# Kernel tuning notes

Hardware: AMD Instinct MI355X
Metric: run time of the kernel (lower is better)

Reference implementation:

```python
import jax, jax.numpy as jnp
import numpy as np

DIM = 8          # per-head dim
ATT_EPS = 1e-15
BN_EPS = 1e-6


def setup_inputs() -> dict:
    key = jax.random.key(0)
    ks = jax.random.split(key, 6)
    B, C, H, W = 8, 256, 64, 64
    td = 256                      # heads * dim = 32 * 8
    return {
        'x':      jax.random.normal(ks[0], (B, C, H, W), jnp.float32),
        'w_qkv':  jax.random.normal(ks[1], (3 * td, C), jnp.float32) * 0.05,
        'w_dw':   jax.random.normal(ks[2], (3 * td, 1, 5, 5), jnp.float32) * 0.05,
        'w_pw':   jax.random.normal(ks[3], (96, 8, 8), jnp.float32) * 0.05,   # (groups, out/g, in/g)
        'w_proj': jax.random.normal(ks[4], (C, 2 * td), jnp.float32) * 0.05,
        'bn_gamma': jnp.ones((C,), jnp.float32),
        'bn_beta':  jnp.zeros((C,), jnp.float32),
        'bn_mean':  jnp.zeros((C,), jnp.float32),
        'bn_var':   jnp.ones((C,), jnp.float32),
    }


def _relu_linear_att(ms, H, W):
    # ms: [B, C, H, W] with C = heads * 3*DIM
    B = ms.shape[0]
    d = DIM
    qkv = ms.reshape(B, -1, 3 * d, H * W).transpose(0, 1, 3, 2)   # [B, h, N, 3d]
    q = jax.nn.relu(qkv[..., :d])
    k = jax.nn.relu(qkv[..., d:2 * d])
    v = qkv[..., 2 * d:]
    v = jnp.pad(v, ((0, 0), (0, 0), (0, 0), (0, 1)), constant_values=1.0)  # ones column
    kv = jnp.einsum('bhnd,bhne->bhde', k, v)                       # [B, h, d, d+1]
    out = jnp.einsum('bhnd,bhde->bhne', q, kv)                     # [B, h, N, d+1]
    out = out[..., :-1] / (out[..., -1:] + ATT_EPS)
    return out.transpose(0, 1, 3, 2).reshape(B, -1, H, W)          # [B, h*d, H, W]


def reference(x, w_qkv, w_dw, w_pw, w_proj, bn_gamma, bn_beta, bn_mean, bn_var):
    B, C, H, W = x.shape
    # 1x1 qkv projection
    qkv = jnp.einsum('oc,bchw->bohw', w_qkv, x)                    # [B, 768, H, W]
    # multiscale aggregation: 5x5 depthwise then grouped 1x1 (groups = 3*heads = 96)
    dw = jax.lax.conv_general_dilated(
        qkv, w_dw, window_strides=(1, 1), padding=[(2, 2), (2, 2)],
        dimension_numbers=('NCHW', 'OIHW', 'NCHW'),
        feature_group_count=qkv.shape[1])
    G, O, I = w_pw.shape
    agg = jnp.einsum('goi,bgihw->bgohw', w_pw,
                     dw.reshape(B, G, I, H, W)).reshape(B, G * O, H, W)
    ms = jnp.concatenate([qkv, agg], axis=1)                       # [B, 1536, H, W]
    att = _relu_linear_att(ms, H, W)                               # [B, 512, H, W]
    # proj: 1x1 conv + BatchNorm (eval mode) + identity activation
    p = jnp.einsum('oc,bchw->bohw', w_proj, att)                   # [B, 256, H, W]
    inv = bn_gamma / jnp.sqrt(bn_var + BN_EPS)
    p = p * inv[None, :, None, None] + (bn_beta - bn_mean * inv)[None, :, None, None]
    return x + p
```

## Files before the change

### kernel.cpp

```cpp
#include <hip/hip_runtime.h>
#include <hip/hip_bf16.h>


#define HW 4096
#define ATT_EPS 1e-15f
#define BN_EPS 1e-6f

typedef __attribute__((ext_vector_type(8))) short short8;
typedef __attribute__((ext_vector_type(4))) short short4v;
typedef __attribute__((ext_vector_type(4))) float f32x4;
typedef __attribute__((ext_vector_type(2))) float f32x2;
typedef __attribute__((ext_vector_type(8))) unsigned short u16x8;
typedef __attribute__((ext_vector_type(4))) unsigned short u16x4;

static __device__ inline short f2bf(float f) {
    union { float f; unsigned u; } v; v.f = f;
    unsigned r = v.u + 0x7fff + ((v.u >> 16) & 1);
    return (short)(r >> 16);
}
static __device__ inline float bf2f(unsigned short u) {
    union { unsigned u; float f; } v; v.u = (unsigned)u << 16; return v.f;
}

static __device__ inline float dpp_shr1(float x) {
    int i = __builtin_bit_cast(int, x);
    int r = __builtin_amdgcn_update_dpp(0, i, 0x111, 0xF, 0xF, true);
    return __builtin_bit_cast(float, r);
}
static __device__ inline float dpp_shl1(float x) {
    int i = __builtin_bit_cast(int, x);
    int r = __builtin_amdgcn_update_dpp(0, i, 0x101, 0xF, 0xF, true);
    return __builtin_bit_cast(float, r);
}

__global__ __launch_bounds__(256) void prep_w(const float* __restrict__ wproj,
                                              unsigned short* __restrict__ wbf) {
    const int i = (blockIdx.x * 256 + threadIdx.x) * 4;
    float4 v = *(const float4*)&wproj[i];
    u16x4 r = {(unsigned short)f2bf(v.x), (unsigned short)f2bf(v.y),
               (unsigned short)f2bf(v.z), (unsigned short)f2bf(v.w)};
    *(u16x4*)&wbf[i] = r;
}

__global__ __launch_bounds__(256) void prep_wq(const float* __restrict__ wqkv,
                                               unsigned short* __restrict__ wqbf) {
    const int i = (blockIdx.x * 256 + threadIdx.x) * 4;
    float4 v = *(const float4*)&wqkv[i];
    u16x4 r = {(unsigned short)f2bf(v.x), (unsigned short)f2bf(v.y),
               (unsigned short)f2bf(v.z), (unsigned short)f2bf(v.w)};
    *(u16x4*)&wqbf[i] = r;
}

__global__ __launch_bounds__(256) void prep_xt(const float* __restrict__ x,
                                               unsigned short* __restrict__ xt) {
    __shared__ unsigned short tl[64][72];
    const int b = blockIdx.z;
    const int c0 = blockIdx.y * 64, n0 = blockIdx.x * 64;
    const int t = threadIdx.x;
    const int nq = t & 15, cl = t >> 4;
#pragma unroll
    for (int p = 0; p < 4; p++) {
        const int c = cl + p * 16;
        float4 v = *(const float4*)&x[((size_t)b * 256 + c0 + c) * HW + n0 + nq * 4];
        tl[nq * 4 + 0][c] = (unsigned short)f2bf(v.x);
        tl[nq * 4 + 1][c] = (unsigned short)f2bf(v.y);
        tl[nq * 4 + 2][c] = (unsigned short)f2bf(v.z);
        tl[nq * 4 + 3][c] = (unsigned short)f2bf(v.w);
    }
    __syncthreads();
#pragma unroll
    for (int k = 0; k < 2; k++) {
        const int slot = t + 256 * k;
        const int nl = slot >> 3, oct = slot & 7;
        u16x8 v = *(const u16x8*)&tl[nl][oct * 8];
        *(u16x8*)&xt[((size_t)b * 4096 + n0 + nl) * 256 + c0 + oct * 8] = v;
    }
}

__global__ __launch_bounds__(256) void qkv_gemm(const unsigned short* __restrict__ xt,
                                                const unsigned short* __restrict__ wqbf,
                                                unsigned short* __restrict__ qkv) {
    __shared__ unsigned short A_l[128 * 40];
    __shared__ unsigned short B_l[128 * 40];
    const int t  = threadIdx.x;
    const int b  = blockIdx.z;
    const int ob = blockIdx.y * 128;
    const int nb = blockIdx.x * 128;
    const int lane = t & 63, wave = t >> 6;
    const int wo = (wave >> 1) * 64, wn = (wave & 1) * 64;
    const int am = lane & 15, ak = lane >> 4;

    const int r0 = t >> 2, c0 = t & 3;
    const unsigned short* asrc = wqbf + (size_t)(ob + r0) * 256 + c0 * 8;
    const unsigned short* bsrc = xt + ((size_t)b * 4096 + nb + r0) * 256 + c0 * 8;

    f32x4 acc[4][4];
#pragma unroll
    for (int s = 0; s < 4; s++)
#pragma unroll
        for (int u = 0; u < 4; u++) acc[s][u] = (f32x4){0.f, 0.f, 0.f, 0.f};

    for (int kb = 0; kb < 256; kb += 32) {
        __syncthreads();
        *(u16x8*)&A_l[r0 * 40 + c0 * 8] = *(const u16x8*)(asrc + kb);
        *(u16x8*)&A_l[(r0 + 64) * 40 + c0 * 8] =
            *(const u16x8*)(asrc + (size_t)64 * 256 + kb);
        *(u16x8*)&B_l[r0 * 40 + c0 * 8] = *(const u16x8*)(bsrc + kb);
        *(u16x8*)&B_l[(r0 + 64) * 40 + c0 * 8] =
            *(const u16x8*)(bsrc + (size_t)64 * 256 + kb);
        __syncthreads();

        short8 af[4], bf[4];
#pragma unroll
        for (int s = 0; s < 4; s++)
            af[s] = *(const short8*)&A_l[(wo + s * 16 + am) * 40 + ak * 8];
#pragma unroll
        for (int u = 0; u < 4; u++)
            bf[u] = *(const short8*)&B_l[(wn + u * 16 + am) * 40 + ak * 8];
#pragma unroll
        for (int s = 0; s < 4; s++)
#pragma unroll
            for (int u = 0; u < 4; u++)
                acc[s][u] = __builtin_amdgcn_mfma_f32_16x16x32_bf16(af[s], bf[u], acc[s][u], 0, 0, 0);
    }

#pragma unroll
    for (int s = 0; s < 4; s++)
#pragma unroll
        for (int u = 0; u < 4; u++)
#pragma unroll
            for (int r = 0; r < 4; r++) {
                const int o = ob + wo + s * 16 + (lane >> 4) * 4 + r;
                const int nn = nb + wn + u * 16 + (lane & 15);
                qkv[((size_t)b * 768 + o) * HW + nn] = (unsigned short)f2bf(acc[s][u][r]);
            }
}

__global__ __launch_bounds__(256, 6) void dw_agg(const unsigned short* __restrict__ qkv,
                                                 const float* __restrict__ wdw,
                                                 const float* __restrict__ wpw,
                                                 unsigned short* __restrict__ agg) {
    __shared__ float tile[4 * 20 * 64];
    const int b = blockIdx.z, g = blockIdx.y;
    const int y0 = blockIdx.x * 16;
    const int t = threadIdx.x;
    const int tx = t & 15, ty = t >> 4;

    const float* wkg = wdw + g * 8 * 25;
    const float* pwg = wpw + g * 64;

    float out[8][4];
#pragma unroll
    for (int o = 0; o < 8; o++)
#pragma unroll
        for (int j = 0; j < 4; j++) out[o][j] = 0.f;

#pragma unroll 1
    for (int half = 0; half < 2; half++) {
        if (half) __syncthreads();
#pragma unroll
        for (int k = 0; k < 3; k++) {
            const int i = t + 256 * k;
            if (i < 640) {
                const int c8 = i & 7, rr = (i >> 3) % 20, ch = i / 160;
                const int y = y0 - 2 + rr;
                u16x8 v = {0, 0, 0, 0, 0, 0, 0, 0};
                if (y >= 0 && y < 64)
                    v = *(const u16x8*)&qkv[((size_t)(b * 768 + g * 8 + half * 4 + ch)) * HW + y * 64 + c8 * 8];
                f32x4 lo = {bf2f(v[0]), bf2f(v[1]), bf2f(v[2]), bf2f(v[3])};
                f32x4 hi = {bf2f(v[4]), bf2f(v[5]), bf2f(v[6]), bf2f(v[7])};
                *(f32x4*)&tile[i * 8]     = lo;
                *(f32x4*)&tile[i * 8 + 4] = hi;
            }
        }
        __syncthreads();

#pragma unroll 1
        for (int ch4 = 0; ch4 < 4; ch4++) {
            const int ch = half * 4 + ch4;
            const float* wkc = wkg + ch * 25;
            float a0 = 0.f, a1 = 0.f, a2 = 0.f, a3 = 0.f;
#pragma unroll
            for (int dy = 0; dy < 5; dy++) {
                const int off = ch4 * 1280 + (ty + dy) * 64 + tx * 4;
                f32x4 C = *(const f32x4*)&tile[off];
                float win[8];
                win[0] = dpp_shr1(C[2]);
                win[1] = dpp_shr1(C[3]);
                win[2] = C[0]; win[3] = C[1];
                win[4] = C[2]; win[5] = C[3];
                win[6] = dpp_shl1(C[0]);
                win[7] = dpp_shl1(C[1]);
#pragma unroll
                for (int dx = 0; dx < 5; dx++) {
                    const float wv = wkc[dy * 5 + dx];
                    a0 += wv * win[dx + 0];
                    a1 += wv * win[dx + 1];
                    a2 += wv * win[dx + 2];
                    a3 += wv * win[dx + 3];
                }
            }
#pragma unroll
            for (int o = 0; o < 8; o++) {
                const float wv = pwg[o * 8 + ch];
                out[o][0] += wv * a0; out[o][1] += wv * a1;
                out[o][2] += wv * a2; out[o][3] += wv * a3;
            }
        }
    }

#pragma unroll
    for (int o = 0; o < 8; o++) {
        u16x4 rv = {(unsigned short)f2bf(out[o][0]), (unsigned short)f2bf(out[o][1]),
                    (unsigned short)f2bf(out[o][2]), (unsigned short)f2bf(out[o][3])};
        *(u16x4*)&agg[((size_t)(b * 768 + g * 8 + o)) * HW + (y0 + ty) * 64 + tx * 4] = rv;
    }
}

__global__ __launch_bounds__(256) void kv_pass(const unsigned short* __restrict__ qkv,
                                               const unsigned short* __restrict__ agg,
                                               float* __restrict__ kvpart) {
    const int t = threadIdx.x;
    const int w = t >> 6, lane = t & 63;
    const int hp = blockIdx.x * 4 + w;
    const int b = blockIdx.y, c = blockIdx.z;
    const int h0 = hp * 2, h1 = h0 + 1;
    const unsigned short* buf = (h0 < 32) ? qkv : agg;
    const int cb0 = (h0 & 31) * 24, cb1 = (h1 & 31) * 24;

    const int row = lane & 15, kgrp = lane >> 4;
    const int n0 = c * 256 + kgrp * 8;

    const int chA = (row < 8) ? (cb0 + 8 + row) : (cb1 + row);
    const unsigned short* ap = buf + ((size_t)b * 768 + chA) * HW + n0;

    const bool bload = (row < 8);
    const unsigned short* bp0 = buf + ((size_t)b * 768 + cb0 + 16 + (row & 7)) * HW + n0;
    const unsigned short* bp1 = buf + ((size_t)b * 768 + cb1 + 16 + (row & 7)) * HW + n0;
    const short cfill = (row == 8) ? (short)0x3F80 : (short)0;
    const short8 bconst = {cfill, cfill, cfill, cfill, cfill, cfill, cfill, cfill};

    f32x4 acc0 = {0.f, 0.f, 0.f, 0.f};
    f32x4 acc1 = {0.f, 0.f, 0.f, 0.f};

#pragma unroll
    for (int i = 0; i < 8; i++) {
        u16x8 av = *(const u16x8*)(ap + i * 32);
        short8 b0 = bload ? *(const short8*)(bp0 + i * 32) : bconst;
        short8 b1 = bload ? *(const short8*)(bp1 + i * 32) : bconst;
        short8 ar;
#pragma unroll
        for (int j = 0; j < 8; j++)
            ar[j] = (short)((av[j] & 0x8000) ? 0 : av[j]);
        acc0 = __builtin_amdgcn_mfma_f32_16x16x32_bf16(ar, b0, acc0, 0, 0, 0);
        acc1 = __builtin_amdgcn_mfma_f32_16x16x32_bf16(ar, b1, acc1, 0, 0, 0);
    }

    if (row <= 8) {
        float* kp;
        f32x4 a;
        int dbase;
        if (kgrp < 2) {
            kp = kvpart + (size_t)c * 36864 + (size_t)(b * 64 + h0) * 72;
            a = acc0; dbase = kgrp * 4;
        } else {
            kp = kvpart + (size_t)c * 36864 + (size_t)(b * 64 + h1) * 72;
            a = acc1; dbase = (kgrp - 2) * 4;
        }
#pragma unroll
        for (int r = 0; r < 4; r++)
            kp[(dbase + r) * 9 + row] = a[r];
    }
}

__global__ __launch_bounds__(256) void kv_red(const float* __restrict__ kvpart,
                                              float* __restrict__ kvout) {
    const int i = blockIdx.x * 256 + threadIdx.x;
    float s = 0.f;
#pragma unroll
    for (int c = 0; c < 16; c++) s += kvpart[(size_t)c * 36864 + i];
    kvout[i] = s;
}

__global__ __launch_bounds__(256) void att_pass(const unsigned short* __restrict__ qkv,
                                                const unsigned short* __restrict__ agg,
                                                const float* __restrict__ kvbuf,
                                                unsigned short* __restrict__ att_f) {
    const int h = blockIdx.y, b = blockIdx.z;
    const int t = threadIdx.x;
    const float* kvp = kvbuf + ((size_t)(b * 64 + h)) * 72;

    float kvr[72];
#pragma unroll
    for (int i = 0; i < 18; i++) {
        f32x4 v = *(const f32x4*)&kvp[i * 4];
        kvr[i * 4 + 0] = v[0]; kvr[i * 4 + 1] = v[1];
        kvr[i * 4 + 2] = v[2]; kvr[i * 4 + 3] = v[3];
    }

    const unsigned short* buf = (h < 32) ? qkv : agg;
    const int cbase = (h & 31) * 24;
    const int n0 = (blockIdx.x * 256 + t) * 8;
    const unsigned short* qp = buf + ((size_t)b * 768 + cbase) * HW + n0;

    float q[8][8];
#pragma unroll
    for (int d = 0; d < 8; d++) {
        u16x8 v = *(const u16x8*)&qp[(size_t)d * HW];
#pragma unroll
        for (int j = 0; j < 8; j++) q[d][j] = fmaxf(bf2f(v[j]), 0.f);
    }

    unsigned short* op = att_f + (((size_t)(b * 64 + h)) * HW + n0) * 8;
#pragma unroll
    for (int j = 0; j < 8; j++) {
        float num[9];
#pragma unroll
        for (int e = 0; e < 9; e++) num[e] = 0.f;
#pragma unroll
        for (int d = 0; d < 8; d++) {
            const float qv = q[d][j];
#pragma unroll
            for (int e = 0; e < 9; e++) num[e] += qv * kvr[d * 9 + e];
        }
        const float rden = 1.f / (num[8] + ATT_EPS);
        u16x8 r;
#pragma unroll
        for (int e = 0; e < 8; e++) r[e] = (unsigned short)f2bf(num[e] * rden);
        *(u16x8*)&op[j * 8] = r;
    }
}

__global__ __launch_bounds__(256) void proj_gemm(const unsigned short* __restrict__ wbf,
                                                 const unsigned short* __restrict__ att_f,
                                                 const float* __restrict__ gamma,
                                                 const float* __restrict__ beta,
                                                 const float* __restrict__ mean,
                                                 const float* __restrict__ var,
                                                 const float* __restrict__ x,
                                                 float* __restrict__ out) {
    const int t  = threadIdx.x;
    const int b  = blockIdx.z;
    const int ob = blockIdx.y * 128;
    const int nb = blockIdx.x * 128;
    const int lane = t & 63, wave = t >> 6;
    const int wo = (wave >> 1) * 64, wn = (wave & 1) * 64;

    const int am = lane & 15, ak = lane >> 4;
    const unsigned short* ap0 = wbf + (size_t)(ob + wo + am) * 512 + ak * 8;
    const unsigned short* bp0 = att_f +
        (((size_t)b * 64 + ak) * HW + nb + wn + am) * 8;

    f32x4 acc[4][4];
#pragma unroll
    for (int s = 0; s < 4; s++)
#pragma unroll
        for (int u = 0; u < 4; u++) acc[s][u] = (f32x4){0.f, 0.f, 0.f, 0.f};

    for (int kb = 0; kb < 512; kb += 32) {
        short8 af[4], bf[4];
#pragma unroll
        for (int s = 0; s < 4; s++)
            af[s] = *(const short8*)(ap0 + (size_t)s * 16 * 512 + kb);
#pragma unroll
        for (int u = 0; u < 4; u++)
            bf[u] = *(const short8*)(bp0 + ((size_t)(kb >> 3) * HW + u * 16) * 8);
#pragma unroll
        for (int s = 0; s < 4; s++)
#pragma unroll
            for (int u = 0; u < 4; u++)
                acc[s][u] = __builtin_amdgcn_mfma_f32_16x16x32_bf16(af[s], bf[u], acc[s][u], 0, 0, 0);
    }

#pragma unroll
    for (int s = 0; s < 4; s++) {
        const int o_base = ob + wo + s * 16 + (lane >> 4) * 4;
#pragma unroll
        for (int r = 0; r < 4; r++) {
            const int o = o_base + r;
            const float inv = gamma[o] * rsqrtf(var[o] + BN_EPS);
            const float sh  = beta[o] - mean[o] * inv;
#pragma unroll
            for (int u = 0; u < 4; u++) {
                const int n = nb + wn + u * 16 + (lane & 15);
                const size_t idx = ((size_t)b * 256 + o) * HW + n;
                out[idx] = x[idx] + acc[s][u][r] * inv + sh;
            }
        }
    }
}

extern "C" void kernel_launch(void* const* d_in, const int* in_sizes, int n_in,
                              void* d_out, int out_size, void* d_ws, size_t ws_size,
                              hipStream_t stream) {
    const float* x      = (const float*)d_in[0];
    const float* w_qkv  = (const float*)d_in[1];
    const float* w_dw   = (const float*)d_in[2];
    const float* w_pw   = (const float*)d_in[3];
    const float* w_proj = (const float*)d_in[4];
    const float* gamma  = (const float*)d_in[5];
    const float* beta   = (const float*)d_in[6];
    const float* mean   = (const float*)d_in[7];
    const float* var    = (const float*)d_in[8];
    float* out = (float*)d_out;

    unsigned short* qkv  = (unsigned short*)d_ws;
    unsigned short* agg  = qkv + (size_t)25165824;
    unsigned short* attf = agg + (size_t)25165824;
    unsigned short* wbf  = attf + (size_t)16777216;
    float* kvb = (float*)(wbf + (size_t)131072);
    float* kvpart = (float*)attf;
    unsigned short* wqbf = attf + (size_t)4194304;
    unsigned short* xt   = agg;

    prep_w  <<<dim3(128),       256, 0, stream>>>(w_proj, wbf);
    prep_wq <<<dim3(192),       256, 0, stream>>>(w_qkv, wqbf);
    prep_xt <<<dim3(64, 4, 8),  256, 0, stream>>>(x, xt);
    qkv_gemm<<<dim3(32, 6, 8),  256, 0, stream>>>(xt, wqbf, qkv);
    dw_agg  <<<dim3(4, 96, 8),  256, 0, stream>>>(qkv, w_dw, w_pw, agg);
    kv_pass <<<dim3(8, 8, 16),  256, 0, stream>>>(qkv, agg, kvpart);
    kv_red  <<<dim3(144),       256, 0, stream>>>(kvpart, kvb);
    att_pass<<<dim3(2, 64, 8),  256, 0, stream>>>(qkv, agg, kvb, attf);
    proj_gemm<<<dim3(32, 2, 8), 256, 0, stream>>>(wbf, attf,
                                                  gamma, beta, mean, var, x, out);
}
```

Baseline: 224.5 us.

## Prefetch global tiles into registers in qkv GEMM and dw_agg, merge weight prep

```diff
diff --git a/kernel.cpp b/kernel.cpp
--- a/kernel.cpp
+++ b/kernel.cpp
@@ -33,22 +33,20 @@
     return __builtin_bit_cast(float, r);
 }
 
-__global__ __launch_bounds__(256) void prep_w(const float* __restrict__ wproj,
-                                              unsigned short* __restrict__ wbf) {
-    const int i = (blockIdx.x * 256 + threadIdx.x) * 4;
-    float4 v = *(const float4*)&wproj[i];
+__global__ __launch_bounds__(256) void prep_wb(const float* __restrict__ wproj,
+                                               const float* __restrict__ wqkv,
+                                               unsigned short* __restrict__ wbf,
+                                               unsigned short* __restrict__ wqbf) {
+    const int bid = blockIdx.x;
+    const float* src;
+    unsigned short* dst;
+    int i;
+    if (bid < 128) { src = wproj; dst = wbf;  i = (bid * 256 + threadIdx.x) * 4; }
+    else           { src = wqkv;  dst = wqbf; i = ((bid - 128) * 256 + threadIdx.x) * 4; }
+    float4 v = *(const float4*)&src[i];
     u16x4 r = {(unsigned short)f2bf(v.x), (unsigned short)f2bf(v.y),
                (unsigned short)f2bf(v.z), (unsigned short)f2bf(v.w)};
-    *(u16x4*)&wbf[i] = r;
-}
-
-__global__ __launch_bounds__(256) void prep_wq(const float* __restrict__ wqkv,
-                                               unsigned short* __restrict__ wqbf) {
-    const int i = (blockIdx.x * 256 + threadIdx.x) * 4;
-    float4 v = *(const float4*)&wqkv[i];
-    u16x4 r = {(unsigned short)f2bf(v.x), (unsigned short)f2bf(v.y),
-               (unsigned short)f2bf(v.z), (unsigned short)f2bf(v.w)};
-    *(u16x4*)&wqbf[i] = r;
+    *(u16x4*)&dst[i] = r;
 }
 
 __global__ __launch_bounds__(256) void prep_xt(const float* __restrict__ x,
@@ -100,15 +98,25 @@
 #pragma unroll
         for (int u = 0; u < 4; u++) acc[s][u] = (f32x4){0.f, 0.f, 0.f, 0.f};
 
+    u16x8 pa0, pa1, pb0, pb1;
+#define QFETCH(KB)                                                             \
+    {                                                                          \
+        pa0 = *(const u16x8*)(asrc + (KB));                                    \
+        pa1 = *(const u16x8*)(asrc + (size_t)64 * 256 + (KB));                 \
+        pb0 = *(const u16x8*)(bsrc + (KB));                                    \
+        pb1 = *(const u16x8*)(bsrc + (size_t)64 * 256 + (KB));                 \
+    }
+
+    QFETCH(0)
     for (int kb = 0; kb < 256; kb += 32) {
         __syncthreads();
-        *(u16x8*)&A_l[r0 * 40 + c0 * 8] = *(const u16x8*)(asrc + kb);
-        *(u16x8*)&A_l[(r0 + 64) * 40 + c0 * 8] =
-            *(const u16x8*)(asrc + (size_t)64 * 256 + kb);
-        *(u16x8*)&B_l[r0 * 40 + c0 * 8] = *(const u16x8*)(bsrc + kb);
-        *(u16x8*)&B_l[(r0 + 64) * 40 + c0 * 8] =
-            *(const u16x8*)(bsrc + (size_t)64 * 256 + kb);
+        *(u16x8*)&A_l[r0 * 40 + c0 * 8]        = pa0;
+        *(u16x8*)&A_l[(r0 + 64) * 40 + c0 * 8] = pa1;
+        *(u16x8*)&B_l[r0 * 40 + c0 * 8]        = pb0;
+        *(u16x8*)&B_l[(r0 + 64) * 40 + c0 * 8] = pb1;
         __syncthreads();
+
+        if (kb + 32 < 256) QFETCH(kb + 32)
 
         short8 af[4], bf[4];
 #pragma unroll
@@ -123,6 +131,7 @@
             for (int u = 0; u < 4; u++)
                 acc[s][u] = __builtin_amdgcn_mfma_f32_16x16x32_bf16(af[s], bf[u], acc[s][u], 0, 0, 0);
     }
+#undef QFETCH
 
 #pragma unroll
     for (int s = 0; s < 4; s++)
@@ -136,7 +145,7 @@
             }
 }
 
-__global__ __launch_bounds__(256, 6) void dw_agg(const unsigned short* __restrict__ qkv,
+__global__ __launch_bounds__(256, 4) void dw_agg(const unsigned short* __restrict__ qkv,
                                                  const float* __restrict__ wdw,
                                                  const float* __restrict__ wpw,
                                                  unsigned short* __restrict__ agg) {
@@ -155,6 +164,24 @@
 #pragma unroll
         for (int j = 0; j < 4; j++) out[o][j] = 0.f;
 
+    u16x8 pf0, pf1, pf2;
+#define DWFETCH(HALF)                                                          \
+    {                                                                          \
+        _Pragma("unroll")                                                      \
+        for (int k = 0; k < 3; k++) {                                          \
+            const int i = t + 256 * k;                                         \
+            u16x8 v = {0, 0, 0, 0, 0, 0, 0, 0};                                \
+            if (i < 640) {                                                     \
+                const int c8 = i & 7, rr = (i >> 3) % 20, ch = i / 160;        \
+                const int y = y0 - 2 + rr;                                     \
+                if (y >= 0 && y < 64)                                          \
+                    v = *(const u16x8*)&qkv[((size_t)(b * 768 + g * 8 + (HALF) * 4 + ch)) * HW + y * 64 + c8 * 8]; \
+            }                                                                  \
+            if (k == 0) pf0 = v; else if (k == 1) pf1 = v; else pf2 = v;       \
+        }                                                                      \
+    }
+
+    DWFETCH(0)
 #pragma unroll 1
     for (int half = 0; half < 2; half++) {
         if (half) __syncthreads();
@@ -162,11 +189,7 @@
         for (int k = 0; k < 3; k++) {
             const int i = t + 256 * k;
             if (i < 640) {
-                const int c8 = i & 7, rr = (i >> 3) % 20, ch = i / 160;
-                const int y = y0 - 2 + rr;
-                u16x8 v = {0, 0, 0, 0, 0, 0, 0, 0};
-                if (y >= 0 && y < 64)
-                    v = *(const u16x8*)&qkv[((size_t)(b * 768 + g * 8 + half * 4 + ch)) * HW + y * 64 + c8 * 8];
+                u16x8 v = (k == 0) ? pf0 : (k == 1) ? pf1 : pf2;
                 f32x4 lo = {bf2f(v[0]), bf2f(v[1]), bf2f(v[2]), bf2f(v[3])};
                 f32x4 hi = {bf2f(v[4]), bf2f(v[5]), bf2f(v[6]), bf2f(v[7])};
                 *(f32x4*)&tile[i * 8]     = lo;
@@ -174,8 +197,9 @@
             }
         }
         __syncthreads();
-
-#pragma unroll 1
+        if (half == 0) DWFETCH(1)
+
+#pragma unroll 2
         for (int ch4 = 0; ch4 < 4; ch4++) {
             const int ch = half * 4 + ch4;
             const float* wkc = wkg + ch * 25;
@@ -208,6 +232,7 @@
             }
         }
     }
+#undef DWFETCH
 
 #pragma unroll
     for (int o = 0; o < 8; o++) {
@@ -413,8 +438,7 @@
     unsigned short* wqbf = attf + (size_t)4194304;
     unsigned short* xt   = agg;
 
-    prep_w  <<<dim3(128),       256, 0, stream>>>(w_proj, wbf);
-    prep_wq <<<dim3(192),       256, 0, stream>>>(w_qkv, wqbf);
+    prep_wb <<<dim3(320),       256, 0, stream>>>(w_proj, w_qkv, wbf, wqbf);
     prep_xt <<<dim3(64, 4, 8),  256, 0, stream>>>(x, xt);
     qkv_gemm<<<dim3(32, 6, 8),  256, 0, stream>>>(xt, wqbf, qkv);
     dw_agg  <<<dim3(4, 96, 8),  256, 0, stream>>>(qkv, w_dw, w_pw, agg);
```

New measurement: 220.0 us. 1.02x faster.
